# Optimization experiments

Hardware: AMD Instinct MI355X
Metric: run time of the kernel (lower is better)

Reference implementation:

```python
import jax, jax.numpy as jnp
import numpy as np

B, T, I, U, O = 128, 2048, 128, 256, 128
KILL = (3, 7)  # kill_neuron list: zero these hidden units after each step


def setup_inputs() -> dict:
    key = jax.random.key(0)
    ks = jax.random.split(key, 7)
    s = 1.0 / np.sqrt(U)  # torch nn.RNN / nn.Linear default uniform init bound
    u = lambda k, sh: jax.random.uniform(k, sh, jnp.float32, -s, s)
    return {
        "x": jax.random.normal(ks[0], (B, T, I), jnp.float32),
        "W_ih": u(ks[1], (U, I)),
        "W_hh": u(ks[2], (U, U)),
        "b_ih": u(ks[3], (U,)),
        "b_hh": u(ks[4], (U,)),
        "W_fc": u(ks[5], (O, U)),
        "b_fc": u(ks[6], (O,)),
    }


def reference(x, W_ih, W_hh, b_ih, b_hh, W_fc, b_fc):
    units = W_hh.shape[0]
    mask = jnp.ones((units,), x.dtype).at[jnp.array(KILL)].set(0.0)
    h0 = jnp.zeros((x.shape[0], units), x.dtype)  # initial_state=None -> zeros
    # Precompute input projection for all timesteps: [B,T,U] -> scan xs [T,B,U]
    x_proj = jnp.einsum('bti,ui->btu', x, W_ih) + b_ih + b_hh

    def step(h, xt):  # xt: [B,U]
        h_raw = jnp.tanh(xt + h @ W_hh.T)   # rnn output 'temp' (unmasked)
        h_masked = h_raw * mask             # kill_neuron applied to carried hidden
        return h_masked, (h_raw, h_masked)

    _, (h_raw_seq, h_masked_seq) = jax.lax.scan(step, h0, jnp.swapaxes(x_proj, 0, 1))
    # readout is fc(temp) i.e. applied to the UNMASKED per-step output
    readouts = jnp.einsum('tbu,ou->bto', h_raw_seq, W_fc) + b_fc  # [B,T,O]
    hs = jnp.swapaxes(h_masked_seq, 0, 1)  # [B,T,U] (masked hidden states)
    return readouts, hs
```

## Files before the change

### kernel.cpp

```cpp
#include <hip/hip_runtime.h>
#include <math.h>

#define BB 128
#define TT 2048
#define II 128
#define UU 256
#define OO 128

typedef __attribute__((ext_vector_type(8))) short bf16x8;
typedef __attribute__((ext_vector_type(4))) float f32x4;

#define MFMA16(a, b, cacc) __builtin_amdgcn_mfma_f32_16x16x32_bf16(a, b, cacc, 0, 0, 0)

__device__ __forceinline__ void bar_lds() {
    __builtin_amdgcn_sched_barrier(0);
    asm volatile("s_waitcnt lgkmcnt(0)" ::: "memory");
    __builtin_amdgcn_s_barrier();
    __builtin_amdgcn_sched_barrier(0);
}

__device__ __forceinline__ short f2bf(float f) {
    unsigned u = __float_as_uint(f);
    unsigned r = (u + 0x7FFFu + ((u >> 16) & 1u)) >> 16;
    return (short)r;
}

__device__ __forceinline__ bf16x8 loadf8(const float* p) {
    float4 va = *reinterpret_cast<const float4*>(p);
    float4 vb = *reinterpret_cast<const float4*>(p + 4);
    bf16x8 v;
    v[0] = f2bf(va.x); v[1] = f2bf(va.y); v[2] = f2bf(va.z); v[3] = f2bf(va.w);
    v[4] = f2bf(vb.x); v[5] = f2bf(vb.y); v[6] = f2bf(vb.z); v[7] = f2bf(vb.w);
    return v;
}

__global__ __launch_bounds__(512, 2) void k_fused(
    const float* __restrict__ x, const float* __restrict__ Wih,
    const float* __restrict__ Whh, const float* __restrict__ bih,
    const float* __restrict__ bhh, const float* __restrict__ Wfc,
    const float* __restrict__ bfc, float* __restrict__ outR,
    float* __restrict__ outH)
{
    __shared__ __align__(16) short hbuf[2 * 256];
    __shared__ __align__(16) short xbuf[4 * 128];
    __shared__ __align__(16) float hside[2][2];

    const int tid = threadIdx.x;
    const int b = blockIdx.x;
    const int w = tid >> 6;
    const int lane = tid & 63;
    const int g = lane >> 4;
    const int c = lane & 15;
    const int q = g & 1;
    const int uxp = w * 32 + q * 16 + c;
    const int ow  = w * 16 + c;
    const bool hswr  = (g < 2);
    const bool ldswr = (g >= 2);
    const bool kill = (uxp == 3) || (uxp == 7);

    bf16x8 bq[2][8];
    bf16x8 wi[2][4];
    bf16x8 wf[8];
    #pragma unroll
    for (int q2 = 0; q2 < 2; ++q2) {
        const int ub = w * 32 + q2 * 16 + c;
        #pragma unroll
        for (int kt = 0; kt < 8; ++kt)
            bq[q2][kt] = loadf8(&Whh[(size_t)ub * UU + kt * 32 + g * 8]);
        #pragma unroll
        for (int kt = 0; kt < 4; ++kt)
            wi[q2][kt] = loadf8(&Wih[(size_t)ub * II + kt * 32 + g * 8]);
    }
    #pragma unroll
    for (int kt = 0; kt < 8; ++kt)
        wf[kt] = loadf8(&Wfc[(size_t)ow * UU + kt * 32 + g * 8]);
    const float biasu = bih[uxp] + bhh[uxp];
    const float bfc_s = bfc[ow];
    const float wfc3 = Wfc[(size_t)ow * UU + 3];
    const float wfc7 = Wfc[(size_t)ow * UU + 7];

    if (tid < 256) reinterpret_cast<int*>(hbuf)[tid] = 0;
    if (tid >= 256 && tid < 260)
        reinterpret_cast<float*>(hside)[tid - 256] = 0.f;

    const float* xb = x + (size_t)b * (size_t)TT * II;
    const int xl = tid & 31;
    if (tid < 96) {
        int slot = tid >> 5;
        float4 v = *reinterpret_cast<const float4*>(xb + slot * II + xl * 4);
        short4 s4 = { f2bf(v.x), f2bf(v.y), f2bf(v.z), f2bf(v.w) };
        *reinterpret_cast<short4*>(&xbuf[slot * 128 + xl * 4]) = s4;
    }
    float4 xr = {0.f, 0.f, 0.f, 0.f};
    if (tid < 32)
        xr = *reinterpret_cast<const float4*>(xb + 3 * II + xl * 4);
    __syncthreads();

    auto xproj = [&](int slot) -> float {
        f32x4 xa0 = {0.f,0.f,0.f,0.f}, xa1 = {0.f,0.f,0.f,0.f};
        #pragma unroll
        for (int kt = 0; kt < 4; ++kt) {
            bf16x8 ax = *reinterpret_cast<const bf16x8*>(
                &xbuf[slot * 128 + kt * 32 + g * 8]);
            xa0 = MFMA16(ax, wi[0][kt], xa0);
            xa1 = MFMA16(ax, wi[1][kt], xa1);
        }
        return (q ? xa1[0] : xa0[0]) + biasu;
    };

    float xpv = xproj(0);
    float xpn = xproj(1);

    float* hsrow = outH + (size_t)b * (size_t)TT * UU;
    float* rorow = outR + (size_t)b * (size_t)TT * OO;

    auto step = [&](int t, int p) {
        if (tid < 32) {
            int ws = (t + 3) & 3;
            short4 s4 = { f2bf(xr.x), f2bf(xr.y), f2bf(xr.z), f2bf(xr.w) };
            *reinterpret_cast<short4*>(&xbuf[ws * 128 + xl * 4]) = s4;
            int tl = t + 4; tl = (tl < TT) ? tl : (TT - 1);
            xr = *reinterpret_cast<const float4*>(xb + (size_t)tl * II + xl * 4);
        }
        bf16x8 af[8];
        #pragma unroll
        for (int kt = 0; kt < 8; ++kt)
            af[kt] = *reinterpret_cast<const bf16x8*>(
                &hbuf[p * 256 + kt * 32 + g * 8]);
        float hr3 = hside[p][0], hr7 = hside[p][1];
        f32x4 r00 = {0.f,0.f,0.f,0.f}, r01 = {0.f,0.f,0.f,0.f};
        f32x4 r10 = {0.f,0.f,0.f,0.f}, r11 = {0.f,0.f,0.f,0.f};
        #pragma unroll
        for (int kt = 0; kt < 8; kt += 2) {
            r00 = MFMA16(af[kt],     bq[0][kt],     r00);
            r10 = MFMA16(af[kt],     bq[1][kt],     r10);
            r01 = MFMA16(af[kt + 1], bq[0][kt + 1], r01);
            r11 = MFMA16(af[kt + 1], bq[1][kt + 1], r11);
        }
        f32x4 o0 = {0.f,0.f,0.f,0.f}, o1 = {0.f,0.f,0.f,0.f};
        #pragma unroll
        for (int kt = 0; kt < 8; kt += 2) {
            o0 = MFMA16(af[kt],     wf[kt],     o0);
            o1 = MFMA16(af[kt + 1], wf[kt + 1], o1);
        }
        float xpn2 = xproj((t + 2) & 3);
        float Dres = q ? (r10[0] + r11[0]) : (r00[0] + r01[0]);
        float s = Dres + xpv;
        float hr = 1.0f - 2.0f / (__expf(2.0f * s) + 1.0f);
        if (hswr) hsrow[(size_t)t * UU + uxp] = kill ? 0.f : hr;
        float ro = (o0[0] + o1[0]) + hr3 * wfc3 + hr7 * wfc7 + bfc_s;
        if (t > 0 && g == 0) rorow[(size_t)(t - 1) * OO + ow] = ro;
        if (ldswr) {
            hbuf[(p ^ 1) * 256 + uxp] = kill ? (short)0 : f2bf(hr);
            if (w == 0 && g == 2) {
                if (c == 3) hside[p ^ 1][0] = hr;
                if (c == 7) hside[p ^ 1][1] = hr;
            }
        }
        bar_lds();
        xpv = xpn; xpn = xpn2;
    };
    for (int t = 0; t < TT; t += 2) { step(t, 0); step(t + 1, 1); }

    {
        bf16x8 af[8];
        #pragma unroll
        for (int kt = 0; kt < 8; ++kt)
            af[kt] = *reinterpret_cast<const bf16x8*>(&hbuf[kt * 32 + g * 8]);
        float hr3 = hside[0][0], hr7 = hside[0][1];
        f32x4 o0 = {0.f,0.f,0.f,0.f}, o1 = {0.f,0.f,0.f,0.f};
        #pragma unroll
        for (int kt = 0; kt < 8; kt += 2) {
            o0 = MFMA16(af[kt],     wf[kt],     o0);
            o1 = MFMA16(af[kt + 1], wf[kt + 1], o1);
        }
        float ro = (o0[0] + o1[0]) + hr3 * wfc3 + hr7 * wfc7 + bfc_s;
        if (g == 0) rorow[(size_t)(TT - 1) * OO + ow] = ro;
    }
}

extern "C" void kernel_launch(void* const* d_in, const int* in_sizes, int n_in,
                              void* d_out, int out_size, void* d_ws, size_t ws_size,
                              hipStream_t stream) {
    const float* x   = (const float*)d_in[0];
    const float* Wih = (const float*)d_in[1];
    const float* Whh = (const float*)d_in[2];
    const float* bih = (const float*)d_in[3];
    const float* bhh = (const float*)d_in[4];
    const float* Wfc = (const float*)d_in[5];
    const float* bfc = (const float*)d_in[6];
    float* outR = (float*)d_out;
    float* outH = outR + (size_t)BB * TT * OO;

    k_fused<<<128, 512, 0, stream>>>(x, Wih, Whh, bih, bhh, Wfc, bfc, outR, outH);
}
```

Measured before the change: 1.448 ms.

## Warp-specialize recurrence and projection/readout into separate wave groups

Doubles the block to 1024 threads and splits the waves into two groups. Eight waves run only the recurrent W_hh MFMA and tanh on the critical path. The other eight compute the input projection two steps ahead into an LDS ring and compute the fc readout. This removes the projection and readout MFMAs from the serial per-step chain, at the cost of more waves sharing one barrier per step and extra LDS traffic for the projected inputs.

```diff
diff --git a/kernel.cpp b/kernel.cpp
--- a/kernel.cpp
+++ b/kernel.cpp
@@ -34,7 +34,7 @@
     return v;
 }
 
-__global__ __launch_bounds__(512, 2) void k_fused(
+__global__ __launch_bounds__(1024, 4) void k_fused(
     const float* __restrict__ x, const float* __restrict__ Wih,
     const float* __restrict__ Whh, const float* __restrict__ bih,
     const float* __restrict__ bhh, const float* __restrict__ Wfc,
@@ -43,6 +43,7 @@
 {
     __shared__ __align__(16) short hbuf[2 * 256];
     __shared__ __align__(16) short xbuf[4 * 128];
+    __shared__ __align__(16) float xpring[4 * 256];
     __shared__ __align__(16) float hside[2][2];
 
     const int tid = threadIdx.x;
@@ -52,130 +53,147 @@
     const int g = lane >> 4;
     const int c = lane & 15;
     const int q = g & 1;
-    const int uxp = w * 32 + q * 16 + c;
-    const int ow  = w * 16 + c;
-    const bool hswr  = (g < 2);
-    const bool ldswr = (g >= 2);
-    const bool kill = (uxp == 3) || (uxp == 7);
-
-    bf16x8 bq[2][8];
-    bf16x8 wi[2][4];
-    bf16x8 wf[8];
-    #pragma unroll
-    for (int q2 = 0; q2 < 2; ++q2) {
-        const int ub = w * 32 + q2 * 16 + c;
-        #pragma unroll
-        for (int kt = 0; kt < 8; ++kt)
-            bq[q2][kt] = loadf8(&Whh[(size_t)ub * UU + kt * 32 + g * 8]);
-        #pragma unroll
-        for (int kt = 0; kt < 4; ++kt)
-            wi[q2][kt] = loadf8(&Wih[(size_t)ub * II + kt * 32 + g * 8]);
-    }
-    #pragma unroll
-    for (int kt = 0; kt < 8; ++kt)
-        wf[kt] = loadf8(&Wfc[(size_t)ow * UU + kt * 32 + g * 8]);
-    const float biasu = bih[uxp] + bhh[uxp];
-    const float bfc_s = bfc[ow];
-    const float wfc3 = Wfc[(size_t)ow * UU + 3];
-    const float wfc7 = Wfc[(size_t)ow * UU + 7];
-
-    if (tid < 256) reinterpret_cast<int*>(hbuf)[tid] = 0;
-    if (tid >= 256 && tid < 260)
-        reinterpret_cast<float*>(hside)[tid - 256] = 0.f;
 
     const float* xb = x + (size_t)b * (size_t)TT * II;
-    const int xl = tid & 31;
-    if (tid < 96) {
-        int slot = tid >> 5;
-        float4 v = *reinterpret_cast<const float4*>(xb + slot * II + xl * 4);
-        short4 s4 = { f2bf(v.x), f2bf(v.y), f2bf(v.z), f2bf(v.w) };
-        *reinterpret_cast<short4*>(&xbuf[slot * 128 + xl * 4]) = s4;
-    }
-    float4 xr = {0.f, 0.f, 0.f, 0.f};
-    if (tid < 32)
-        xr = *reinterpret_cast<const float4*>(xb + 3 * II + xl * 4);
-    __syncthreads();
-
-    auto xproj = [&](int slot) -> float {
-        f32x4 xa0 = {0.f,0.f,0.f,0.f}, xa1 = {0.f,0.f,0.f,0.f};
-        #pragma unroll
-        for (int kt = 0; kt < 4; ++kt) {
-            bf16x8 ax = *reinterpret_cast<const bf16x8*>(
-                &xbuf[slot * 128 + kt * 32 + g * 8]);
-            xa0 = MFMA16(ax, wi[0][kt], xa0);
-            xa1 = MFMA16(ax, wi[1][kt], xa1);
-        }
-        return (q ? xa1[0] : xa0[0]) + biasu;
-    };
-
-    float xpv = xproj(0);
-    float xpn = xproj(1);
-
     float* hsrow = outH + (size_t)b * (size_t)TT * UU;
     float* rorow = outR + (size_t)b * (size_t)TT * OO;
 
-    auto step = [&](int t, int p) {
-        if (tid < 32) {
-            int ws = (t + 3) & 3;
-            short4 s4 = { f2bf(xr.x), f2bf(xr.y), f2bf(xr.z), f2bf(xr.w) };
-            *reinterpret_cast<short4*>(&xbuf[ws * 128 + xl * 4]) = s4;
-            int tl = t + 4; tl = (tl < TT) ? tl : (TT - 1);
-            xr = *reinterpret_cast<const float4*>(xb + (size_t)tl * II + xl * 4);
-        }
-        bf16x8 af[8];
+    if (w < 8) {
+        const int uxp = w * 32 + q * 16 + c;
+        const bool kill = (uxp == 3) || (uxp == 7);
+        bf16x8 bq[2][8];
+        #pragma unroll
+        for (int q2 = 0; q2 < 2; ++q2) {
+            const int ub = w * 32 + q2 * 16 + c;
+            #pragma unroll
+            for (int kt = 0; kt < 8; ++kt)
+                bq[q2][kt] = loadf8(&Whh[(size_t)ub * UU + kt * 32 + g * 8]);
+        }
+        if (tid < 256) reinterpret_cast<int*>(hbuf)[tid] = 0;
+        if (tid < 4) reinterpret_cast<float*>(hside)[tid] = 0.f;
+        bar_lds();
+        bar_lds();
+        for (int t = 0; t < TT; ++t) {
+            const int p = t & 1;
+            float xpv = xpring[(t & 3) * 256 + uxp];
+            bf16x8 af[8];
+            #pragma unroll
+            for (int kt = 0; kt < 8; ++kt)
+                af[kt] = *reinterpret_cast<const bf16x8*>(
+                    &hbuf[p * 256 + kt * 32 + g * 8]);
+            f32x4 r00 = {0.f,0.f,0.f,0.f}, r01 = {0.f,0.f,0.f,0.f};
+            f32x4 r10 = {0.f,0.f,0.f,0.f}, r11 = {0.f,0.f,0.f,0.f};
+            #pragma unroll
+            for (int kt = 0; kt < 8; kt += 2) {
+                r00 = MFMA16(af[kt],     bq[0][kt],     r00);
+                r10 = MFMA16(af[kt],     bq[1][kt],     r10);
+                r01 = MFMA16(af[kt + 1], bq[0][kt + 1], r01);
+                r11 = MFMA16(af[kt + 1], bq[1][kt + 1], r11);
+            }
+            float Dres = q ? (r10[0] + r11[0]) : (r00[0] + r01[0]);
+            float s = Dres + xpv;
+            float hr = 1.0f - 2.0f / (__expf(2.0f * s) + 1.0f);
+            if (g < 2) {
+                hsrow[(size_t)t * UU + uxp] = kill ? 0.f : hr;
+            } else {
+                hbuf[(p ^ 1) * 256 + uxp] = kill ? (short)0 : f2bf(hr);
+                if (w == 0 && g == 2) {
+                    if (c == 3) hside[p ^ 1][0] = hr;
+                    if (c == 7) hside[p ^ 1][1] = hr;
+                }
+            }
+            bar_lds();
+        }
+    } else {
+        const int hw = w - 8;
+        const int ow  = hw * 16 + c;
+        const int uxh = hw * 32 + q * 16 + c;
+        bf16x8 wi[2][4], wf[8];
+        #pragma unroll
+        for (int q2 = 0; q2 < 2; ++q2) {
+            const int ub = hw * 32 + q2 * 16 + c;
+            #pragma unroll
+            for (int kt = 0; kt < 4; ++kt)
+                wi[q2][kt] = loadf8(&Wih[(size_t)ub * II + kt * 32 + g * 8]);
+        }
         #pragma unroll
         for (int kt = 0; kt < 8; ++kt)
-            af[kt] = *reinterpret_cast<const bf16x8*>(
-                &hbuf[p * 256 + kt * 32 + g * 8]);
-        float hr3 = hside[p][0], hr7 = hside[p][1];
-        f32x4 r00 = {0.f,0.f,0.f,0.f}, r01 = {0.f,0.f,0.f,0.f};
-        f32x4 r10 = {0.f,0.f,0.f,0.f}, r11 = {0.f,0.f,0.f,0.f};
-        #pragma unroll
-        for (int kt = 0; kt < 8; kt += 2) {
-            r00 = MFMA16(af[kt],     bq[0][kt],     r00);
-            r10 = MFMA16(af[kt],     bq[1][kt],     r10);
-            r01 = MFMA16(af[kt + 1], bq[0][kt + 1], r01);
-            r11 = MFMA16(af[kt + 1], bq[1][kt + 1], r11);
-        }
-        f32x4 o0 = {0.f,0.f,0.f,0.f}, o1 = {0.f,0.f,0.f,0.f};
-        #pragma unroll
-        for (int kt = 0; kt < 8; kt += 2) {
-            o0 = MFMA16(af[kt],     wf[kt],     o0);
-            o1 = MFMA16(af[kt + 1], wf[kt + 1], o1);
-        }
-        float xpn2 = xproj((t + 2) & 3);
-        float Dres = q ? (r10[0] + r11[0]) : (r00[0] + r01[0]);
-        float s = Dres + xpv;
-        float hr = 1.0f - 2.0f / (__expf(2.0f * s) + 1.0f);
-        if (hswr) hsrow[(size_t)t * UU + uxp] = kill ? 0.f : hr;
-        float ro = (o0[0] + o1[0]) + hr3 * wfc3 + hr7 * wfc7 + bfc_s;
-        if (t > 0 && g == 0) rorow[(size_t)(t - 1) * OO + ow] = ro;
-        if (ldswr) {
-            hbuf[(p ^ 1) * 256 + uxp] = kill ? (short)0 : f2bf(hr);
-            if (w == 0 && g == 2) {
-                if (c == 3) hside[p ^ 1][0] = hr;
-                if (c == 7) hside[p ^ 1][1] = hr;
-            }
-        }
-        bar_lds();
-        xpv = xpn; xpn = xpn2;
-    };
-    for (int t = 0; t < TT; t += 2) { step(t, 0); step(t + 1, 1); }
-
-    {
-        bf16x8 af[8];
-        #pragma unroll
-        for (int kt = 0; kt < 8; ++kt)
-            af[kt] = *reinterpret_cast<const bf16x8*>(&hbuf[kt * 32 + g * 8]);
-        float hr3 = hside[0][0], hr7 = hside[0][1];
-        f32x4 o0 = {0.f,0.f,0.f,0.f}, o1 = {0.f,0.f,0.f,0.f};
-        #pragma unroll
-        for (int kt = 0; kt < 8; kt += 2) {
-            o0 = MFMA16(af[kt],     wf[kt],     o0);
-            o1 = MFMA16(af[kt + 1], wf[kt + 1], o1);
-        }
-        float ro = (o0[0] + o1[0]) + hr3 * wfc3 + hr7 * wfc7 + bfc_s;
-        if (g == 0) rorow[(size_t)(TT - 1) * OO + ow] = ro;
+            wf[kt] = loadf8(&Wfc[(size_t)ow * UU + kt * 32 + g * 8]);
+        const float biasu = bih[uxh] + bhh[uxh];
+        const float bfc_s = bfc[ow];
+        const float wfc3 = Wfc[(size_t)ow * UU + 3];
+        const float wfc7 = Wfc[(size_t)ow * UU + 7];
+        const int xl = lane & 31;
+        float4 xr = {0.f, 0.f, 0.f, 0.f};
+        if (hw < 2) {
+            int slot = hw * 2 + (lane >> 5);
+            float4 v = *reinterpret_cast<const float4*>(xb + slot * II + xl * 4);
+            short4 s4 = { f2bf(v.x), f2bf(v.y), f2bf(v.z), f2bf(v.w) };
+            *reinterpret_cast<short4*>(&xbuf[slot * 128 + xl * 4]) = s4;
+        }
+        if (hw == 0 && lane < 32)
+            xr = *reinterpret_cast<const float4*>(xb + 4 * II + xl * 4);
+        bar_lds();
+        #pragma unroll
+        for (int s0 = 0; s0 < 2; ++s0) {
+            f32x4 xa0 = {0.f,0.f,0.f,0.f}, xa1 = {0.f,0.f,0.f,0.f};
+            #pragma unroll
+            for (int kt = 0; kt < 4; ++kt) {
+                bf16x8 ax = *reinterpret_cast<const bf16x8*>(
+                    &xbuf[s0 * 128 + kt * 32 + g * 8]);
+                xa0 = MFMA16(ax, wi[0][kt], xa0);
+                xa1 = MFMA16(ax, wi[1][kt], xa1);
+            }
+            if (g < 2) xpring[s0 * 256 + uxh] = (q ? xa1[0] : xa0[0]) + biasu;
+        }
+        bar_lds();
+        for (int t = 0; t < TT; ++t) {
+            const int p = t & 1;
+            if (hw == 0 && lane < 32) {
+                short4 s4 = { f2bf(xr.x), f2bf(xr.y), f2bf(xr.z), f2bf(xr.w) };
+                *reinterpret_cast<short4*>(&xbuf[((t + 4) & 3) * 128 + xl * 4]) = s4;
+                int tl = t + 5; tl = (tl < TT) ? tl : (TT - 1);
+                xr = *reinterpret_cast<const float4*>(xb + (size_t)tl * II + xl * 4);
+            }
+            bf16x8 af[8];
+            #pragma unroll
+            for (int kt = 0; kt < 8; ++kt)
+                af[kt] = *reinterpret_cast<const bf16x8*>(
+                    &hbuf[p * 256 + kt * 32 + g * 8]);
+            f32x4 o0 = {0.f,0.f,0.f,0.f}, o1 = {0.f,0.f,0.f,0.f};
+            #pragma unroll
+            for (int kt = 0; kt < 8; kt += 2) {
+                o0 = MFMA16(af[kt],     wf[kt],     o0);
+                o1 = MFMA16(af[kt + 1], wf[kt + 1], o1);
+            }
+            float hr3 = hside[p][0], hr7 = hside[p][1];
+            float ro = (o0[0] + o1[0]) + hr3 * wfc3 + hr7 * wfc7 + bfc_s;
+            if (t > 0 && g == 0) rorow[(size_t)(t - 1) * OO + ow] = ro;
+            f32x4 xa0 = {0.f,0.f,0.f,0.f}, xa1 = {0.f,0.f,0.f,0.f};
+            #pragma unroll
+            for (int kt = 0; kt < 4; ++kt) {
+                bf16x8 ax = *reinterpret_cast<const bf16x8*>(
+                    &xbuf[((t + 2) & 3) * 128 + kt * 32 + g * 8]);
+                xa0 = MFMA16(ax, wi[0][kt], xa0);
+                xa1 = MFMA16(ax, wi[1][kt], xa1);
+            }
+            if (g < 2) xpring[((t + 2) & 3) * 256 + uxh] = (q ? xa1[0] : xa0[0]) + biasu;
+            bar_lds();
+        }
+        {
+            bf16x8 af[8];
+            #pragma unroll
+            for (int kt = 0; kt < 8; ++kt)
+                af[kt] = *reinterpret_cast<const bf16x8*>(&hbuf[kt * 32 + g * 8]);
+            f32x4 o0 = {0.f,0.f,0.f,0.f}, o1 = {0.f,0.f,0.f,0.f};
+            #pragma unroll
+            for (int kt = 0; kt < 8; kt += 2) {
+                o0 = MFMA16(af[kt],     wf[kt],     o0);
+                o1 = MFMA16(af[kt + 1], wf[kt + 1], o1);
+            }
+            float ro = (o0[0] + o1[0]) + hside[0][0] * wfc3 + hside[0][1] * wfc7 + bfc_s;
+            if (g == 0) rorow[(size_t)(TT - 1) * OO + ow] = ro;
+        }
     }
 }
 
@@ -192,5 +210,5 @@
     float* outR = (float*)d_out;
     float* outH = outR + (size_t)BB * TT * OO;
 
-    k_fused<<<128, 512, 0, stream>>>(x, Wih, Whh, bih, bhh, Wfc, bfc, outR, outH);
-}
+    k_fused<<<128, 1024, 0, stream>>>(x, Wih, Whh, bih, bhh, Wfc, bfc, outR, outH);
+}
```

Result: no change. 1.426 ms (-1.5%).
